# Optimization experiments

Measured on AMD Instinct MI355X. Metric: run time of the kernel, lower is better.

Reference implementation:

```python
import jax, jax.numpy as jnp
import numpy as np

H = 4096
NH = 32
HD = 128
FF = 14336
EPS = 1e-6


def _rmsnorm(x, w):
    xf = x.astype(jnp.float32)
    var = jnp.mean(xf * xf, axis=-1, keepdims=True)
    return (w * (xf * jax.lax.rsqrt(var + EPS))).astype(x.dtype)


def setup_inputs() -> dict:
    key = jax.random.key(0)
    ks = jax.random.split(key, 16)
    S = 2048
    def lin(k, fan_in, shape):
        bound = 1.0 / np.sqrt(fan_in)
        return jax.random.uniform(k, shape, jnp.float32, -bound, bound)
    return {
        "hidden_states": jax.random.normal(ks[0], (S, H), jnp.float32),
        "position_ids": jnp.arange(S, dtype=jnp.int64),
        "wq": lin(ks[1], H, (NH * HD, H)), "bq": lin(ks[2], H, (NH * HD,)),
        "wk": lin(ks[3], H, (NH * HD, H)), "bk": lin(ks[4], H, (NH * HD,)),
        "wv": lin(ks[5], H, (NH * HD, H)), "bv": lin(ks[6], H, (NH * HD,)),
        "wo": lin(ks[7], H, (H, H)), "bo": lin(ks[8], H, (H,)),
        "w_gate": lin(ks[9], H, (FF, H)),
        "w_up": lin(ks[10], H, (FF, H)),
        "w_down": lin(ks[11], FF, (H, FF)),
        "ln1_w": jnp.ones((H,), jnp.float32),
        "ln2_w": jnp.ones((H,), jnp.float32),
    }


def reference(hidden_states, position_ids, wq, bq, wk, bk, wv, bv, wo, bo,
              w_gate, w_up, w_down, ln1_w, ln2_w):
    S = hidden_states.shape[0]
    # --- attention block ---
    x = _rmsnorm(hidden_states, ln1_w)
    q = (x @ wq.T + bq).reshape(S, NH, HD)
    k = (x @ wk.T + bk).reshape(S, NH, HD)
    v = (x @ wv.T + bv).reshape(S, NH, HD)
    scale = 1.0 / np.sqrt(HD)
    scores = jnp.einsum('qhd,khd->hqk', q.astype(jnp.float32),
                        k.astype(jnp.float32)) * scale
    causal = jnp.tril(jnp.ones((S, S), bool))  # decoder causal mask
    scores = jnp.where(causal[None, :, :], scores, -jnp.inf)
    probs = jax.nn.softmax(scores, axis=-1)
    h = jnp.einsum('hqk,khd->qhd', probs, v.astype(jnp.float32))
    attn_out = h.reshape(S, NH * HD).astype(hidden_states.dtype) @ wo.T + bo
    h1 = hidden_states + attn_out
    # --- SwiGLU MLP block ---
    y = _rmsnorm(h1, ln2_w)
    mlp = (jax.nn.silu(y @ w_gate.T) * (y @ w_up.T)) @ w_down.T
    return h1 + mlp
```

## Files before the change

### kernel.cpp

```cpp
#include <hip/hip_runtime.h>
#include <math.h>

#define H_DIM 4096
#define NHEAD 32
#define HD 128
#define FF_DIM 14336

typedef unsigned short u16;
typedef __attribute__((ext_vector_type(8))) short bf16x8;
typedef __attribute__((ext_vector_type(4))) float f32x4;

typedef const __attribute__((address_space(1))) void* gas_ptr;
typedef __attribute__((address_space(3))) void* las_ptr;

__device__ __forceinline__ void gload_lds16(const void* g, void* l) {
  __builtin_amdgcn_global_load_lds((gas_ptr)g, (las_ptr)l, 16, 0, 0);
}

__device__ __forceinline__ u16 f32_to_bf16(float f) {
  unsigned int u = __float_as_uint(f);
  u = (u + 0x7FFFu + ((u >> 16) & 1u)) >> 16;
  return (u16)u;
}
__device__ __forceinline__ float bf16_to_f32(u16 x) {
  return __uint_as_float(((unsigned int)x) << 16);
}

__global__ void f2b_kernel(const float* __restrict__ in, u16* __restrict__ out, long n4) {
  long i = (long)blockIdx.x * blockDim.x + threadIdx.x;
  long stride = (long)gridDim.x * blockDim.x;
  for (; i < n4; i += stride) {
    float4 v = reinterpret_cast<const float4*>(in)[i];
    ushort4 o;
    o.x = f32_to_bf16(v.x); o.y = f32_to_bf16(v.y);
    o.z = f32_to_bf16(v.z); o.w = f32_to_bf16(v.w);
    reinterpret_cast<ushort4*>(out)[i] = o;
  }
}

__global__ void bias_concat_kernel(const float* __restrict__ a, const float* __restrict__ b,
                                   const float* __restrict__ c, float* __restrict__ out) {
  int i = blockIdx.x * blockDim.x + threadIdx.x;
  float v;
  if (i < 4096) v = a[i];
  else if (i < 8192) v = b[i - 4096];
  else v = c[i - 8192];
  out[i] = v;
}

__global__ void rmsnorm_kernel(const float* __restrict__ in, const float* __restrict__ w,
                               u16* __restrict__ out) {
  int row = blockIdx.x;
  int tid = threadIdx.x;
  const float4* x4 = reinterpret_cast<const float4*>(in + (size_t)row * H_DIM);
  float4 vv[4];
  float ss = 0.f;
#pragma unroll
  for (int it = 0; it < 4; ++it) {
    float4 v = x4[tid + it * 256];
    vv[it] = v;
    ss += v.x * v.x + v.y * v.y + v.z * v.z + v.w * v.w;
  }
#pragma unroll
  for (int off = 1; off < 64; off <<= 1) ss += __shfl_xor(ss, off);
  __shared__ float part[4];
  if ((tid & 63) == 0) part[tid >> 6] = ss;
  __syncthreads();
  float tot = part[0] + part[1] + part[2] + part[3];
  float rinv = rsqrtf(tot * (1.0f / H_DIM) + 1e-6f);
  const float4* w4 = reinterpret_cast<const float4*>(w);
  u16* orow = out + (size_t)row * H_DIM;
#pragma unroll
  for (int it = 0; it < 4; ++it) {
    float4 v = vv[it];
    float4 wv = w4[tid + it * 256];
    ushort4 o;
    o.x = f32_to_bf16(v.x * rinv * wv.x);
    o.y = f32_to_bf16(v.y * rinv * wv.y);
    o.z = f32_to_bf16(v.z * rinv * wv.z);
    o.w = f32_to_bf16(v.w * rinv * wv.w);
    reinterpret_cast<ushort4*>(orow)[tid + it * 256] = o;
  }
}

enum { EPI_QKV = 0, EPI_O = 1, EPI_SILU = 2, EPI_MUL = 3, EPI_PART = 4 };

template <int EPI, bool SPLIT>
__global__ __launch_bounds__(512, 2) void gemm256(
    const u16* __restrict__ A, const u16* __restrict__ B, void* __restrict__ outp,
    const float* __restrict__ bias, const void* __restrict__ extra,
    int M, int N, int K, int kLen) {
  __shared__ __align__(16) u16 As[2][256 * 64];
  __shared__ __align__(16) u16 Bs[2][256 * 64];
  const int tid = threadIdx.x;
  const int wid = tid >> 6, lane = tid & 63;
  const int lg = lane >> 4, li = lane & 15;
  const int wr = (wid >> 2) << 7;
  const int wc = (wid & 3) << 6;

  const int nbm = M >> 8, nbn = N >> 8;
  const int nb = nbm * nbn;
  int wg = (blockIdx.x & 7) * (gridDim.x >> 3) + (blockIdx.x >> 3);
  int s = 0;
  if (SPLIT) { s = wg / nb; wg -= s * nb; }
  const int m0 = (wg % nbm) << 8, n0 = (wg / nbm) << 8;
  const int kB = SPLIT ? s * kLen : 0;
  const int NT = kLen >> 6;

  const int r8 = tid >> 3;
  const int sl = ((tid & 7) ^ (r8 & 7)) << 3;
  const u16* sA[2][2];
  const u16* sB[2][2];
  int ldo[2][2];
#pragma unroll
  for (int P = 0; P < 2; ++P)
#pragma unroll
    for (int h = 0; h < 2; ++h) {
      int lr = P * 128 + h * 64 + r8;
      int ra = (lr & 63) | ((lr >> 1) & 64) | ((lr << 1) & 128);
      int rb = (lr & 31) | ((lr & 96) << 1) | ((lr & 128) >> 2);
      sA[P][h] = A + (size_t)(m0 + ra) * K + kB + sl;
      sB[P][h] = B + (size_t)(n0 + rb) * K + kB + sl;
      ldo[P][h] = (P * 128 + h * 64 + (wid << 3)) << 6;
    }

  auto stageA = [&](int P, int d, int ko) {
#pragma unroll
    for (int h = 0; h < 2; ++h)
      gload_lds16(sA[P][h] + ko, (void*)(&As[d][ldo[P][h]]));
  };
  auto stageB = [&](int P, int d, int ko) {
#pragma unroll
    for (int h = 0; h < 2; ++h)
      gload_lds16(sB[P][h] + ko, (void*)(&Bs[d][ldo[P][h]]));
  };

  bf16x8 a[4][2], b[4][2];
  f32x4 acc[8][4] = {};
  const int s20 = (lg ^ (li & 7)) << 3;
  const int s21 = ((4 + lg) ^ (li & 7)) << 3;

  auto ldA = [&](int d, int set) {
#pragma unroll
    for (int i = 0; i < 4; ++i) {
      int g = wr + set * 64 + i * 16;
      int lb = (g & 63) | ((g >> 1) & 64) | ((g << 1) & 128);
      const u16* base = &As[d][(lb + li) << 6];
      a[i][0] = *reinterpret_cast<const bf16x8*>(base + s20);
      a[i][1] = *reinterpret_cast<const bf16x8*>(base + s21);
    }
  };
  auto ldB = [&](int d, int set) {
#pragma unroll
    for (int jj = 0; jj < 2; ++jj) {
      int hh = wc + (set * 2 + jj) * 16;
      int lb = ((hh & 32) << 2) | ((hh & 192) >> 1) | (hh & 31);
      const u16* base = &Bs[d][(lb + li) << 6];
      b[set * 2 + jj][0] = *reinterpret_cast<const bf16x8*>(base + s20);
      b[set * 2 + jj][1] = *reinterpret_cast<const bf16x8*>(base + s21);
    }
  };
  auto mm = [&](int iset, int jset) {
    __builtin_amdgcn_s_setprio(1);
#pragma unroll
    for (int i = 0; i < 4; ++i)
#pragma unroll
      for (int jj = 0; jj < 2; ++jj)
#pragma unroll
        for (int kk = 0; kk < 2; ++kk)
          acc[iset * 4 + i][jset * 2 + jj] = __builtin_amdgcn_mfma_f32_16x16x32_bf16(
              a[i][kk], b[jset * 2 + jj][kk], acc[iset * 4 + i][jset * 2 + jj], 0, 0, 0);
    __builtin_amdgcn_s_setprio(0);
  };

  stageA(0, 0, 0); stageB(0, 0, 0); stageB(1, 0, 0); stageA(1, 0, 0);
  if (NT > 1) {
    stageA(0, 1, 64); stageB(0, 1, 64); stageB(1, 1, 64); stageA(1, 1, 64);
    asm volatile("s_waitcnt vmcnt(8)" ::: "memory");
  } else {
    asm volatile("s_waitcnt vmcnt(0)" ::: "memory");
  }
  __builtin_amdgcn_s_barrier();

  for (int t = 0; t < NT; ++t) {
    int d = t & 1;
    bool pf = (t + 2) < NT;
    int ko = (t + 2) << 6;
    ldB(d, 0); ldA(d, 0);
    __builtin_amdgcn_s_barrier();
    mm(0, 0);
    __builtin_amdgcn_s_barrier();
    ldB(d, 1);
    if (pf) { stageA(0, d, ko); stageB(0, d, ko); }
    __builtin_amdgcn_s_barrier();
    mm(0, 1);
    __builtin_amdgcn_s_barrier();
    ldA(d, 1);
    if (pf) stageB(1, d, ko);
    __builtin_amdgcn_s_barrier();
    mm(1, 0);
    __builtin_amdgcn_s_barrier();
    if (pf) {
      stageA(1, d, ko);
      asm volatile("s_waitcnt vmcnt(6)" ::: "memory");
    } else {
      asm volatile("s_waitcnt vmcnt(0)" ::: "memory");
    }
    __builtin_amdgcn_s_barrier();
    mm(1, 1);
    __builtin_amdgcn_s_barrier();
  }

#pragma unroll
  for (int i = 0; i < 8; ++i) {
#pragma unroll
    for (int j = 0; j < 4; ++j) {
      int col = n0 + wc + j * 16 + li;
      float bv = 0.f;
      if (EPI == EPI_QKV || EPI == EPI_O) bv = bias[col];
      if (EPI == EPI_PART && bias != nullptr && s == 0) bv = bias[col];
#pragma unroll
      for (int r = 0; r < 4; ++r) {
        int row = m0 + wr + i * 16 + lg * 4 + r;
        float v = acc[i][j][r] + bv;
        size_t idx = (size_t)row * N + col;
        if (EPI == EPI_QKV) {
          ((u16*)outp)[idx] = f32_to_bf16(v);
        } else if (EPI == EPI_O) {
          const float* res = (const float*)extra;
          ((float*)outp)[idx] = res[idx] + v;
        } else if (EPI == EPI_SILU) {
          float sv = v / (1.f + __expf(-v));
          ((u16*)outp)[idx] = f32_to_bf16(sv);
        } else if (EPI == EPI_MUL) {
          const u16* sg = (const u16*)extra;
          ((u16*)outp)[idx] = f32_to_bf16(v * bf16_to_f32(sg[idx]));
        } else {
          ((float*)outp)[(size_t)s * M * N + idx] = v;
        }
      }
    }
  }
}

__global__ void reduce_down(const float* __restrict__ p, const float* __restrict__ res,
                            float* __restrict__ out, long n4, long str4) {
  long i = (long)blockIdx.x * blockDim.x + threadIdx.x;
  long st = (long)gridDim.x * blockDim.x;
  for (; i < n4; i += st) {
    float4 h = reinterpret_cast<const float4*>(res)[i];
    float4 p0 = reinterpret_cast<const float4*>(p)[i];
    float4 p1 = reinterpret_cast<const float4*>(p)[i + str4];
    float4 o;
    o.x = h.x + p0.x + p1.x; o.y = h.y + p0.y + p1.y;
    o.z = h.z + p0.z + p1.z; o.w = h.w + p0.w + p1.w;
    reinterpret_cast<float4*>(out)[i] = o;
  }
}

__global__ void transpose_kernel(const u16* __restrict__ in, u16* __restrict__ out,
                                 int S, int ldin) {
  __shared__ __align__(16) u16 t[64][80];
  int sbT = S >> 6;
  int bs = blockIdx.x % sbT, bc = blockIdx.x / sbT;
  int s0 = bs << 6, c0 = bc << 6;
  int tid = threadIdx.x;
  int ir = tid >> 3;
  int jc = (tid & 7) * 8;
#pragma unroll
  for (int h = 0; h < 2; ++h) {
    int sr = ir + h * 32;
    uint4 v = *reinterpret_cast<const uint4*>(in + (size_t)(s0 + sr) * ldin + c0 + jc);
    *reinterpret_cast<uint4*>(&t[sr][jc]) = v;
  }
  __syncthreads();
  int d = tid >> 3;
  int ss = (tid & 7) * 8;
#pragma unroll
  for (int h = 0; h < 2; ++h) {
    int dd = d + h * 32;
    u16 tmp[8];
#pragma unroll
    for (int e = 0; e < 8; ++e) tmp[e] = t[ss + e][dd];
    *reinterpret_cast<uint4*>(out + (size_t)(c0 + dd) * S + s0 + ss) =
        *reinterpret_cast<const uint4*>(tmp);
  }
}

__global__ __launch_bounds__(256) void attn_kernel(
    const u16* __restrict__ q, const u16* __restrict__ k,
    const u16* __restrict__ vt, u16* __restrict__ o, int S, int ldqk) {
  __shared__ __align__(16) u16 plds[4][32 * 64];
  int tid = threadIdx.x, wid = tid >> 6, lane = tid & 63;
  int lg = lane >> 4, li = lane & 15;
  int nwg = gridDim.x;
  int sbid = (blockIdx.x & 7) * (nwg >> 3) + (blockIdx.x >> 3);
  int task = sbid * 4 + wid;
  int pairs = S >> 6;
  int head = task / pairs;
  int pi = task - head * pairs;
  const float scale = 0.08838834764831845f;
  u16* pl = plds[wid];

  for (int tix = 0; tix < 2; ++tix) {
    int qt = tix ? ((S >> 5) - 1 - pi) : pi;
    int q0 = qt << 5;

    bf16x8 aq[2][4];
#pragma unroll
    for (int fi = 0; fi < 2; ++fi) {
      const u16* qrow = q + (size_t)(q0 + fi * 16 + li) * ldqk + head * HD + lg * 8;
#pragma unroll
      for (int ks = 0; ks < 4; ++ks)
        aq[fi][ks] = *reinterpret_cast<const bf16x8*>(qrow + ks * 32);
    }

    f32x4 oacc[2][8] = {};
    float m_run[2][4], l_run[2][4];
#pragma unroll
    for (int fi = 0; fi < 2; ++fi)
#pragma unroll
      for (int r = 0; r < 4; ++r) { m_run[fi][r] = -INFINITY; l_run[fi][r] = 0.f; }

    int nkb = ((q0 + 31) >> 6) + 1;
    for (int kb = 0; kb < nkb; ++kb) {
      int kvbase = kb << 6;
      f32x4 sacc[2][4] = {};
#pragma unroll
      for (int cf = 0; cf < 4; ++cf) {
        const u16* krow = k + (size_t)(kvbase + cf * 16 + li) * ldqk + head * HD + lg * 8;
#pragma unroll
        for (int ks = 0; ks < 4; ++ks) {
          bf16x8 bk = *reinterpret_cast<const bf16x8*>(krow + ks * 32);
          sacc[0][cf] = __builtin_amdgcn_mfma_f32_16x16x32_bf16(aq[0][ks], bk, sacc[0][cf], 0, 0, 0);
          sacc[1][cf] = __builtin_amdgcn_mfma_f32_16x16x32_bf16(aq[1][ks], bk, sacc[1][cf], 0, 0, 0);
        }
      }
      bool bnd = (kvbase + 63) > q0;
      float alpha[2][4];
#pragma unroll
      for (int fi = 0; fi < 2; ++fi) {
#pragma unroll
        for (int r = 0; r < 4; ++r) {
          int row = q0 + fi * 16 + lg * 4 + r;
#pragma unroll
          for (int cf = 0; cf < 4; ++cf) {
            float sv = sacc[fi][cf][r] * scale;
            if (bnd && (kvbase + cf * 16 + li) > row) sv = -INFINITY;
            sacc[fi][cf][r] = sv;
          }
          float mv = fmaxf(fmaxf(sacc[fi][0][r], sacc[fi][1][r]),
                           fmaxf(sacc[fi][2][r], sacc[fi][3][r]));
#pragma unroll
          for (int off = 1; off < 16; off <<= 1) mv = fmaxf(mv, __shfl_xor(mv, off));
          float mnew = fmaxf(m_run[fi][r], mv);
          alpha[fi][r] = __expf(m_run[fi][r] - mnew);
          m_run[fi][r] = mnew;
          float ps = 0.f;
#pragma unroll
          for (int cf = 0; cf < 4; ++cf) {
            float pv = __expf(sacc[fi][cf][r] - mnew);
            sacc[fi][cf][r] = pv;
            ps += pv;
          }
#pragma unroll
          for (int off = 1; off < 16; off <<= 1) ps += __shfl_xor(ps, off);
          l_run[fi][r] = l_run[fi][r] * alpha[fi][r] + ps;
        }
      }
#pragma unroll
      for (int fi = 0; fi < 2; ++fi)
#pragma unroll
        for (int df = 0; df < 8; ++df)
#pragma unroll
          for (int r = 0; r < 4; ++r) oacc[fi][df][r] *= alpha[fi][r];
#pragma unroll
      for (int fi = 0; fi < 2; ++fi)
#pragma unroll
        for (int cf = 0; cf < 4; ++cf)
#pragma unroll
          for (int r = 0; r < 4; ++r) {
            int row = fi * 16 + lg * 4 + r;
            int el = row * 64 + cf * 16 + li;
            pl[el ^ ((row & 7) << 3)] = f32_to_bf16(sacc[fi][cf][r]);
          }
      asm volatile("s_waitcnt lgkmcnt(0)" ::: "memory");
      __builtin_amdgcn_sched_barrier(0);
#pragma unroll
      for (int kk = 0; kk < 2; ++kk) {
        bf16x8 pa[2];
#pragma unroll
        for (int fi = 0; fi < 2; ++fi) {
          int row = fi * 16 + li;
          int el = row * 64 + kk * 32 + lg * 8;
          pa[fi] = *reinterpret_cast<const bf16x8*>(pl + (el ^ ((row & 7) << 3)));
        }
        const u16* vb = vt + kvbase + kk * 32 + lg * 8;
#pragma unroll
        for (int df = 0; df < 8; ++df) {
          bf16x8 bv = *reinterpret_cast<const bf16x8*>(vb + (size_t)(head * HD + df * 16 + li) * S);
          oacc[0][df] = __builtin_amdgcn_mfma_f32_16x16x32_bf16(pa[0], bv, oacc[0][df], 0, 0, 0);
          oacc[1][df] = __builtin_amdgcn_mfma_f32_16x16x32_bf16(pa[1], bv, oacc[1][df], 0, 0, 0);
        }
      }
    }
#pragma unroll
    for (int fi = 0; fi < 2; ++fi)
#pragma unroll
      for (int r = 0; r < 4; ++r) {
        float inv = 1.0f / l_run[fi][r];
        int row = q0 + fi * 16 + lg * 4 + r;
        u16* orow = o + (size_t)row * H_DIM + head * HD;
#pragma unroll
        for (int df = 0; df < 8; ++df)
          orow[df * 16 + li] = f32_to_bf16(oacc[fi][df][r] * inv);
      }
  }
}

extern "C" void kernel_launch(void* const* d_in, const int* in_sizes, int n_in,
                              void* d_out, int out_size, void* d_ws, size_t ws_size,
                              hipStream_t stream) {
  (void)n_in; (void)out_size;
  const float* hidden = (const float*)d_in[0];
  const float* wq = (const float*)d_in[2];
  const float* bq = (const float*)d_in[3];
  const float* wk = (const float*)d_in[4];
  const float* bk = (const float*)d_in[5];
  const float* wv = (const float*)d_in[6];
  const float* bv = (const float*)d_in[7];
  const float* wo = (const float*)d_in[8];
  const float* bo = (const float*)d_in[9];
  const float* wg = (const float*)d_in[10];
  const float* wu = (const float*)d_in[11];
  const float* wd = (const float*)d_in[12];
  const float* ln1 = (const float*)d_in[13];
  const float* ln2 = (const float*)d_in[14];
  float* out = (float*)d_out;

  int S = in_sizes[0] / H_DIM;
  int NQKV = 3 * H_DIM;

  char* ws = (char*)d_ws;
  size_t off = 0;
  auto alloc = [&](size_t bytes) {
    void* p = ws + off;
    off += (bytes + 255) & ~(size_t)255;
    return p;
  };
  u16* wbuf = (u16*)alloc((size_t)FF_DIM * H_DIM * 2);
  u16* xb   = (u16*)alloc((size_t)S * H_DIM * 2);
  u16* qkv  = (u16*)alloc((size_t)S * NQKV * 2);
  u16* vtb  = (u16*)alloc((size_t)S * H_DIM * 2);
  u16* hat  = (u16*)alloc((size_t)S * H_DIM * 2);
  float* h1 = (float*)alloc((size_t)S * H_DIM * 4);
  u16* sg   = (u16*)alloc((size_t)S * FF_DIM * 2);
  u16* tb   = (u16*)alloc((size_t)S * FF_DIM * 2);
  float* bcat = (float*)alloc((size_t)NQKV * 4);
  if (off > ws_size) return;
  float* pbuf = (float*)qkv;

  dim3 b256(256), b512(512);
  long nHH4 = (long)H_DIM * H_DIM / 4;
  long nFH4 = (long)FF_DIM * H_DIM / 4;
  int gQKV3 = (S / 256) * (NQKV / 256);
  int gO    = 2 * (S / 256) * (H_DIM / 256);
  int gFF   = (S / 256) * (FF_DIM / 256);
  int gDW   = 2 * (S / 256) * (H_DIM / 256);
  long n4HH = (long)S * H_DIM / 4;

  rmsnorm_kernel<<<S, b256, 0, stream>>>(hidden, ln1, xb);
  bias_concat_kernel<<<NQKV / 256, b256, 0, stream>>>(bq, bk, bv, bcat);
  f2b_kernel<<<4096, b256, 0, stream>>>(wq, wbuf, nHH4);
  f2b_kernel<<<4096, b256, 0, stream>>>(wk, wbuf + (size_t)H_DIM * H_DIM, nHH4);
  f2b_kernel<<<4096, b256, 0, stream>>>(wv, wbuf + (size_t)2 * H_DIM * H_DIM, nHH4);
  gemm256<EPI_QKV, false><<<gQKV3, b512, 0, stream>>>(xb, wbuf, qkv, bcat, nullptr,
                                                      S, NQKV, H_DIM, H_DIM);
  transpose_kernel<<<(S / 64) * (H_DIM / 64), b256, 0, stream>>>(qkv + 2 * H_DIM, vtb, S, NQKV);
  attn_kernel<<<(NHEAD * (S / 64)) / 4, b256, 0, stream>>>(qkv, qkv + H_DIM, vtb, hat, S, NQKV);
  f2b_kernel<<<4096, b256, 0, stream>>>(wo, wbuf, nHH4);
  gemm256<EPI_PART, true><<<gO, b512, 0, stream>>>(hat, wbuf, pbuf, bo, nullptr,
                                                   S, H_DIM, H_DIM, H_DIM / 2);
  reduce_down<<<2048, b256, 0, stream>>>(pbuf, hidden, h1, n4HH, n4HH);

  rmsnorm_kernel<<<S, b256, 0, stream>>>(h1, ln2, xb);
  f2b_kernel<<<4096, b256, 0, stream>>>(wg, wbuf, nFH4);
  gemm256<EPI_SILU, false><<<gFF, b512, 0, stream>>>(xb, wbuf, sg, nullptr, nullptr,
                                                     S, FF_DIM, H_DIM, H_DIM);
  f2b_kernel<<<4096, b256, 0, stream>>>(wu, wbuf, nFH4);
  gemm256<EPI_MUL, false><<<gFF, b512, 0, stream>>>(xb, wbuf, tb, nullptr, sg,
                                                    S, FF_DIM, H_DIM, H_DIM);
  f2b_kernel<<<4096, b256, 0, stream>>>(wd, wbuf, nFH4);
  gemm256<EPI_PART, true><<<gDW, b512, 0, stream>>>(tb, wbuf, pbuf, nullptr, nullptr,
                                                    S, H_DIM, FF_DIM, FF_DIM / 2);
  reduce_down<<<2048, b256, 0, stream>>>(pbuf, h1, out, n4HH, n4HH);
}
```

Baseline: 1.657 ms.

## Overlap weight bf16 conversions with GEMM and attention via extra blocks

Gives each weight its own bf16 buffer and moves the fp32-to-bf16 weight conversions into extra trailing blocks of the preceding GEMM and attention launches. These blocks convert the next layers' weights while the compute blocks run, which removes the standalone conversion launches from the critical path. The three QKV conversions are also merged into one kernel. This needs more workspace, so the old sequential path is kept as a fallback, and the conversion blocks compete with the compute blocks for bandwidth and CU slots.

```diff
diff --git a/kernel.cpp b/kernel.cpp
--- a/kernel.cpp
+++ b/kernel.cpp
@@ -26,11 +26,32 @@
   return __uint_as_float(((unsigned int)x) << 16);
 }
 
+__device__ __forceinline__ void conv4(const float* __restrict__ in,
+                                      u16* __restrict__ out, long i) {
+  float4 v = reinterpret_cast<const float4*>(in)[i];
+  ushort4 o;
+  o.x = f32_to_bf16(v.x); o.y = f32_to_bf16(v.y);
+  o.z = f32_to_bf16(v.z); o.w = f32_to_bf16(v.w);
+  reinterpret_cast<ushort4*>(out)[i] = o;
+}
+
 __global__ void f2b_kernel(const float* __restrict__ in, u16* __restrict__ out, long n4) {
   long i = (long)blockIdx.x * blockDim.x + threadIdx.x;
   long stride = (long)gridDim.x * blockDim.x;
-  for (; i < n4; i += stride) {
-    float4 v = reinterpret_cast<const float4*>(in)[i];
+  for (; i < n4; i += stride) conv4(in, out, i);
+}
+
+__global__ void f2b3_kernel(const float* __restrict__ a, const float* __restrict__ b,
+                            const float* __restrict__ c, u16* __restrict__ out, long n4each) {
+  long i = (long)blockIdx.x * blockDim.x + threadIdx.x;
+  long st = (long)gridDim.x * blockDim.x;
+  long tot = 3 * n4each;
+  for (; i < tot; i += st) {
+    const float* src; long j;
+    if (i < n4each)            { src = a; j = i; }
+    else if (i < 2 * n4each)   { src = b; j = i - n4each; }
+    else                       { src = c; j = i - 2 * n4each; }
+    float4 v = reinterpret_cast<const float4*>(src)[j];
     ushort4 o;
     o.x = f32_to_bf16(v.x); o.y = f32_to_bf16(v.y);
     o.z = f32_to_bf16(v.z); o.w = f32_to_bf16(v.w);
@@ -85,11 +106,25 @@
 
 enum { EPI_QKV = 0, EPI_O = 1, EPI_SILU = 2, EPI_MUL = 3, EPI_PART = 4 };
 
-template <int EPI, bool SPLIT>
+template <int EPI, bool SPLIT, bool CONV>
 __global__ __launch_bounds__(512, 2) void gemm256(
     const u16* __restrict__ A, const u16* __restrict__ B, void* __restrict__ outp,
     const float* __restrict__ bias, const void* __restrict__ extra,
-    int M, int N, int K, int kLen) {
+    int M, int N, int K, int kLen, int gemmBlocks,
+    const float* __restrict__ c0in, u16* __restrict__ c0out, long c0n4,
+    const float* __restrict__ c1in, u16* __restrict__ c1out, long c1n4) {
+  if (CONV) {
+    int cb = blockIdx.x - gemmBlocks;
+    if (cb >= 0) {
+      long nconv = gridDim.x - gemmBlocks;
+      long base = (long)cb * 512 + threadIdx.x;
+      long st = nconv * 512;
+      for (long i = base; i < c0n4; i += st) conv4(c0in, c0out, i);
+      if (c1in != nullptr)
+        for (long i = base; i < c1n4; i += st) conv4(c1in, c1out, i);
+      return;
+    }
+  }
   __shared__ __align__(16) u16 As[2][256 * 64];
   __shared__ __align__(16) u16 Bs[2][256 * 64];
   const int tid = threadIdx.x;
@@ -100,7 +135,7 @@
 
   const int nbm = M >> 8, nbn = N >> 8;
   const int nb = nbm * nbn;
-  int wg = (blockIdx.x & 7) * (gridDim.x >> 3) + (blockIdx.x >> 3);
+  int wg = (blockIdx.x & 7) * (gemmBlocks >> 3) + (blockIdx.x >> 3);
   int s = 0;
   if (SPLIT) { s = wg / nb; wg -= s * nb; }
   const int m0 = (wg % nbm) << 8, n0 = (wg / nbm) << 8;
@@ -289,12 +324,22 @@
 
 __global__ __launch_bounds__(256) void attn_kernel(
     const u16* __restrict__ q, const u16* __restrict__ k,
-    const u16* __restrict__ vt, u16* __restrict__ o, int S, int ldqk) {
+    const u16* __restrict__ vt, u16* __restrict__ o, int S, int ldqk,
+    int attnBlocks, const float* __restrict__ cin, u16* __restrict__ cout, long cn4) {
+  if (cin != nullptr) {
+    int cb = blockIdx.x - attnBlocks;
+    if (cb >= 0) {
+      long nconv = gridDim.x - attnBlocks;
+      long i = (long)cb * 256 + threadIdx.x;
+      long st = nconv * 256;
+      for (; i < cn4; i += st) conv4(cin, cout, i);
+      return;
+    }
+  }
   __shared__ __align__(16) u16 plds[4][32 * 64];
   int tid = threadIdx.x, wid = tid >> 6, lane = tid & 63;
   int lg = lane >> 4, li = lane & 15;
-  int nwg = gridDim.x;
-  int sbid = (blockIdx.x & 7) * (nwg >> 3) + (blockIdx.x >> 3);
+  int sbid = (blockIdx.x & 7) * (attnBlocks >> 3) + (blockIdx.x >> 3);
   int task = sbid * 4 + wid;
   int pairs = S >> 6;
   int head = task / pairs;
@@ -448,7 +493,6 @@
     off += (bytes + 255) & ~(size_t)255;
     return p;
   };
-  u16* wbuf = (u16*)alloc((size_t)FF_DIM * H_DIM * 2);
   u16* xb   = (u16*)alloc((size_t)S * H_DIM * 2);
   u16* qkv  = (u16*)alloc((size_t)S * NQKV * 2);
   u16* vtb  = (u16*)alloc((size_t)S * H_DIM * 2);
@@ -457,7 +501,14 @@
   u16* sg   = (u16*)alloc((size_t)S * FF_DIM * 2);
   u16* tb   = (u16*)alloc((size_t)S * FF_DIM * 2);
   float* bcat = (float*)alloc((size_t)NQKV * 4);
-  if (off > ws_size) return;
+  u16* wbufQ = (u16*)alloc((size_t)FF_DIM * H_DIM * 2);
+  size_t needSmall = off;
+  u16* wbufO = (u16*)alloc((size_t)H_DIM * H_DIM * 2);
+  u16* wbufG = (u16*)alloc((size_t)FF_DIM * H_DIM * 2);
+  u16* wbufU = (u16*)alloc((size_t)FF_DIM * H_DIM * 2);
+  size_t needBig = off;
+  if (needSmall > ws_size) return;
+  bool big = (needBig <= ws_size);
   float* pbuf = (float*)qkv;
 
   dim3 b256(256), b512(512);
@@ -469,29 +520,64 @@
   int gDW   = 2 * (S / 256) * (H_DIM / 256);
   long n4HH = (long)S * H_DIM / 4;
 
-  rmsnorm_kernel<<<S, b256, 0, stream>>>(hidden, ln1, xb);
-  bias_concat_kernel<<<NQKV / 256, b256, 0, stream>>>(bq, bk, bv, bcat);
-  f2b_kernel<<<4096, b256, 0, stream>>>(wq, wbuf, nHH4);
-  f2b_kernel<<<4096, b256, 0, stream>>>(wk, wbuf + (size_t)H_DIM * H_DIM, nHH4);
-  f2b_kernel<<<4096, b256, 0, stream>>>(wv, wbuf + (size_t)2 * H_DIM * H_DIM, nHH4);
-  gemm256<EPI_QKV, false><<<gQKV3, b512, 0, stream>>>(xb, wbuf, qkv, bcat, nullptr,
-                                                      S, NQKV, H_DIM, H_DIM);
-  transpose_kernel<<<(S / 64) * (H_DIM / 64), b256, 0, stream>>>(qkv + 2 * H_DIM, vtb, S, NQKV);
-  attn_kernel<<<(NHEAD * (S / 64)) / 4, b256, 0, stream>>>(qkv, qkv + H_DIM, vtb, hat, S, NQKV);
-  f2b_kernel<<<4096, b256, 0, stream>>>(wo, wbuf, nHH4);
-  gemm256<EPI_PART, true><<<gO, b512, 0, stream>>>(hat, wbuf, pbuf, bo, nullptr,
-                                                   S, H_DIM, H_DIM, H_DIM / 2);
-  reduce_down<<<2048, b256, 0, stream>>>(pbuf, hidden, h1, n4HH, n4HH);
-
-  rmsnorm_kernel<<<S, b256, 0, stream>>>(h1, ln2, xb);
-  f2b_kernel<<<4096, b256, 0, stream>>>(wg, wbuf, nFH4);
-  gemm256<EPI_SILU, false><<<gFF, b512, 0, stream>>>(xb, wbuf, sg, nullptr, nullptr,
-                                                     S, FF_DIM, H_DIM, H_DIM);
-  f2b_kernel<<<4096, b256, 0, stream>>>(wu, wbuf, nFH4);
-  gemm256<EPI_MUL, false><<<gFF, b512, 0, stream>>>(xb, wbuf, tb, nullptr, sg,
-                                                    S, FF_DIM, H_DIM, H_DIM);
-  f2b_kernel<<<4096, b256, 0, stream>>>(wd, wbuf, nFH4);
-  gemm256<EPI_PART, true><<<gDW, b512, 0, stream>>>(tb, wbuf, pbuf, nullptr, nullptr,
-                                                    S, H_DIM, FF_DIM, FF_DIM / 2);
-  reduce_down<<<2048, b256, 0, stream>>>(pbuf, h1, out, n4HH, n4HH);
-}
+  if (big) {
+    rmsnorm_kernel<<<S, b256, 0, stream>>>(hidden, ln1, xb);
+    bias_concat_kernel<<<NQKV / 256, b256, 0, stream>>>(bq, bk, bv, bcat);
+    f2b3_kernel<<<4096, b256, 0, stream>>>(wq, wk, wv, wbufQ, nHH4);
+    gemm256<EPI_QKV, false, true><<<gQKV3 + 128, b512, 0, stream>>>(
+        xb, wbufQ, qkv, bcat, nullptr, S, NQKV, H_DIM, H_DIM, gQKV3,
+        wo, wbufO, nHH4, wg, wbufG, nFH4);
+    transpose_kernel<<<(S / 64) * (H_DIM / 64), b256, 0, stream>>>(qkv + 2 * H_DIM, vtb, S, NQKV);
+    attn_kernel<<<(NHEAD * (S / 64)) / 4 + 192, b256, 0, stream>>>(
+        qkv, qkv + H_DIM, vtb, hat, S, NQKV, (NHEAD * (S / 64)) / 4, wu, wbufU, nFH4);
+    gemm256<EPI_PART, true, false><<<gO, b512, 0, stream>>>(
+        hat, wbufO, pbuf, bo, nullptr, S, H_DIM, H_DIM, H_DIM / 2, gO,
+        nullptr, nullptr, 0, nullptr, nullptr, 0);
+    reduce_down<<<2048, b256, 0, stream>>>(pbuf, hidden, h1, n4HH, n4HH);
+
+    rmsnorm_kernel<<<S, b256, 0, stream>>>(h1, ln2, xb);
+    gemm256<EPI_SILU, false, true><<<gFF + 96, b512, 0, stream>>>(
+        xb, wbufG, sg, nullptr, nullptr, S, FF_DIM, H_DIM, H_DIM, gFF,
+        wd, wbufQ, nFH4 / 2, nullptr, nullptr, 0);
+    gemm256<EPI_MUL, false, true><<<gFF + 96, b512, 0, stream>>>(
+        xb, wbufU, tb, nullptr, sg, S, FF_DIM, H_DIM, H_DIM, gFF,
+        wd + (size_t)FF_DIM * H_DIM / 2, wbufQ + (size_t)FF_DIM * H_DIM / 2,
+        nFH4 / 2, nullptr, nullptr, 0);
+    gemm256<EPI_PART, true, false><<<gDW, b512, 0, stream>>>(
+        tb, wbufQ, pbuf, nullptr, nullptr, S, H_DIM, FF_DIM, FF_DIM / 2, gDW,
+        nullptr, nullptr, 0, nullptr, nullptr, 0);
+    reduce_down<<<2048, b256, 0, stream>>>(pbuf, h1, out, n4HH, n4HH);
+  } else {
+    u16* wbuf = wbufQ;
+    rmsnorm_kernel<<<S, b256, 0, stream>>>(hidden, ln1, xb);
+    bias_concat_kernel<<<NQKV / 256, b256, 0, stream>>>(bq, bk, bv, bcat);
+    f2b3_kernel<<<4096, b256, 0, stream>>>(wq, wk, wv, wbuf, nHH4);
+    gemm256<EPI_QKV, false, false><<<gQKV3, b512, 0, stream>>>(
+        xb, wbuf, qkv, bcat, nullptr, S, NQKV, H_DIM, H_DIM, gQKV3,
+        nullptr, nullptr, 0, nullptr, nullptr, 0);
+    transpose_kernel<<<(S / 64) * (H_DIM / 64), b256, 0, stream>>>(qkv + 2 * H_DIM, vtb, S, NQKV);
+    attn_kernel<<<(NHEAD * (S / 64)) / 4, b256, 0, stream>>>(
+        qkv, qkv + H_DIM, vtb, hat, S, NQKV, (NHEAD * (S / 64)) / 4,
+        nullptr, nullptr, 0);
+    f2b_kernel<<<4096, b256, 0, stream>>>(wo, wbuf, nHH4);
+    gemm256<EPI_PART, true, false><<<gO, b512, 0, stream>>>(
+        hat, wbuf, pbuf, bo, nullptr, S, H_DIM, H_DIM, H_DIM / 2, gO,
+        nullptr, nullptr, 0, nullptr, nullptr, 0);
+    reduce_down<<<2048, b256, 0, stream>>>(pbuf, hidden, h1, n4HH, n4HH);
+
+    rmsnorm_kernel<<<S, b256, 0, stream>>>(h1, ln2, xb);
+    f2b_kernel<<<4096, b256, 0, stream>>>(wg, wbuf, nFH4);
+    gemm256<EPI_SILU, false, false><<<gFF, b512, 0, stream>>>(
+        xb, wbuf, sg, nullptr, nullptr, S, FF_DIM, H_DIM, H_DIM, gFF,
+        nullptr, nullptr, 0, nullptr, nullptr, 0);
+    f2b_kernel<<<4096, b256, 0, stream>>>(wu, wbuf, nFH4);
+    gemm256<EPI_MUL, false, false><<<gFF, b512, 0, stream>>>(
+        xb, wbuf, tb, nullptr, sg, S, FF_DIM, H_DIM, H_DIM, gFF,
+        nullptr, nullptr, 0, nullptr, nullptr, 0);
+    f2b_kernel<<<4096, b256, 0, stream>>>(wd, wbuf, nFH4);
+    gemm256<EPI_PART, true, false><<<gDW, b512, 0, stream>>>(
+        tb, wbuf, pbuf, nullptr, nullptr, S, H_DIM, FF_DIM, FF_DIM / 2, gDW,
+        nullptr, nullptr, 0, nullptr, nullptr, 0);
+    reduce_down<<<2048, b256, 0, stream>>>(pbuf, h1, out, n4HH, n4HH);
+  }
+}
```

New measurement: 1.813 ms. 9.4% more time.
